# Kernel optimization log

Hardware: AMD Instinct MI355X
Metric: run time of the kernel (lower is better)

## Reference

```python
import jax, jax.numpy as jnp
import numpy as np

B, CQ, CKV, E = 8, 256, 256, 256
H, W = 64, 64
HP, WP = 32, 32


def setup_inputs() -> dict:
    key = jax.random.key(0)
    ks = jax.random.split(key, 6)
    C = jax.random.normal(ks[0], (B, CQ, H, W), dtype=jnp.float32)
    P = jax.random.normal(ks[1], (B, CKV, HP, WP), dtype=jnp.float32)
    # 1x1 conv weights, kaiming-ish scale; stored as [out_ch, in_ch]
    theta_w = jax.random.normal(ks[2], (E, CQ), dtype=jnp.float32) * (1.0 / np.sqrt(CQ))
    phi_w = jax.random.normal(ks[3], (E, CKV), dtype=jnp.float32) * (1.0 / np.sqrt(CKV))
    g_w = jax.random.normal(ks[4], (E, CKV), dtype=jnp.float32) * (1.0 / np.sqrt(CKV))
    out_w = jax.random.normal(ks[5], (CQ, E), dtype=jnp.float32) * (1.0 / np.sqrt(E))
    return {"C": C, "P": P, "theta_w": theta_w, "phi_w": phi_w, "g_w": g_w, "out_w": out_w}


def reference(C, P, theta_w, phi_w, g_w, out_w):
    b, _, h, w = C.shape
    e = theta_w.shape[0]
    # 1x1 convs are channel GEMMs
    theta_C = jnp.einsum('bchw,ec->behw', C, theta_w).reshape(b, e, h * w)   # [B,E,Nq]
    phi_P = jnp.einsum('bchw,ec->behw', P, phi_w).reshape(b, e, -1)          # [B,E,Nkv]
    g_P = jnp.einsum('bchw,ec->behw', P, g_w).reshape(b, e, -1)              # [B,E,Nkv]
    attn = jnp.einsum('ben,bem->bnm', theta_C, phi_P) / (e ** 0.5)           # [B,Nq,Nkv]
    attn = jax.nn.softmax(attn, axis=-1)
    out = jnp.einsum('bem,bnm->ben', g_P, attn).reshape(b, e, h, w)          # [B,E,H,W]
    out = jnp.einsum('behw,ce->bchw', out, out_w)                            # [B,CQ,H,W]
    return jnp.concatenate([C, out], axis=1)
```

## Files before the change

### kernel.cpp

```cpp
#include <hip/hip_runtime.h>


typedef __attribute__((ext_vector_type(8))) short short8;
typedef __attribute__((ext_vector_type(16))) float f32x16;
typedef unsigned short ushort_t;

__device__ __forceinline__ unsigned short f2bf(float f) {
    unsigned int u = __float_as_uint(f);
    u += 0x7FFFu + ((u >> 16) & 1u);
    return (unsigned short)(u >> 16);
}
__device__ __forceinline__ unsigned int pack2bf(float a, float b) {
    return (unsigned int)f2bf(a) | ((unsigned int)f2bf(b) << 16);
}
__device__ __forceinline__ void gload16(const ushort_t* g, ushort_t* l) {
    __builtin_amdgcn_global_load_lds(
        (const __attribute__((address_space(1))) unsigned int*)g,
        (__attribute__((address_space(3))) unsigned int*)l, 16, 0, 0);
}
__device__ __forceinline__ f32x16 zero16() {
    f32x16 z;
#pragma unroll
    for (int i = 0; i < 16; ++i) z[i] = 0.f;
    return z;
}

__global__ __launch_bounds__(256) void prep_w(const float* __restrict__ thw,
                                              const float* __restrict__ phw,
                                              const float* __restrict__ ow,
                                              const float* __restrict__ gw,
                                              ushort_t* __restrict__ thc,
                                              ushort_t* __restrict__ phc,
                                              ushort_t* __restrict__ w2c) {
    int blk = blockIdx.x;
    int t = threadIdx.x;
    if (blk < 64) {
        int which = blk >> 5;
        int e0 = (blk & 31) * 8;
        const float* src = which ? phw : thw;
        ushort_t* dst = which ? phc : thc;
#pragma unroll
        for (int i = 0; i < 8; ++i) {
            int e = e0 + i, c = t;
            int idx = ((((e >> 5) * 16 + (c >> 4)) * 64 + ((c >> 3) & 1) * 32 + (e & 31)) << 3) + (c & 7);
            dst[idx] = f2bf(src[e * 256 + c]);
        }
    } else {
        int c0 = (blk - 64) * 8;
        float acc[8] = {};
        for (int e = 0; e < 256; ++e) {
            float g = gw[e * 256 + t];
#pragma unroll
            for (int i = 0; i < 8; ++i) acc[i] += ow[(c0 + i) * 256 + e] * g;
        }
#pragma unroll
        for (int i = 0; i < 8; ++i) {
            int c = c0 + i, k = t;
            int idx = ((((c >> 5) * 16 + (k >> 4)) * 64 + ((k >> 3) & 1) * 32 + (c & 31)) << 3) + (k & 7);
            w2c[idx] = f2bf(acc[i]);
        }
    }
}

__global__ __launch_bounds__(256, 4) void proj_all(const ushort_t* __restrict__ thc,
                                                   const ushort_t* __restrict__ phc,
                                                   const ushort_t* __restrict__ w2c,
                                                   const float* __restrict__ C,
                                                   const float* __restrict__ P,
                                                   ushort_t* __restrict__ thetaA,
                                                   ushort_t* __restrict__ phiA,
                                                   ushort_t* __restrict__ gVx) {
    __shared__ __align__(16) ushort_t Xc[16384];
    int blk = blockIdx.x;
    int tid = threadIdx.x, lane = tid & 63, wid = tid >> 6;
    int l31 = lane & 31, lh = lane >> 5;
    const int wq = wid & 1, we = wid >> 1;

    int role, b, nt, N;
    const ushort_t* Wc;
    const float* Xg;
    ushort_t* outp;
    float scale = 1.f;
    if (blk < 512) {
        role = 0; b = blk & 7; nt = blk >> 3;
        Wc = thc; Xg = C + (size_t)b * 1048576; outp = thetaA + (size_t)b * 1048576;
        N = 4096; scale = 1.4426950408889634f / 16.0f;
    } else if (blk < 640) {
        int r = blk - 512; role = 1; b = r & 7; nt = r >> 3;
        Wc = phc; Xg = P + (size_t)b * 262144; outp = phiA + (size_t)b * 262144;
        N = 1024;
    } else {
        int r = blk - 640; role = 2; b = r & 7; nt = r >> 3;
        Wc = w2c; Xg = P + (size_t)b * 262144; outp = gVx + (size_t)b * 262144;
        N = 1024;
    }

    {
        const float* Xb = Xg + nt * 64;
        const int q = lane;
        const int sq = q >> 5, sl = q & 31;
#pragma unroll
        for (int it = 0; it < 16; ++it) {
            int ch0 = wid * 4 + it * 16;
            float v0 = Xb[(size_t)(ch0 + 0) * N + q];
            float v1 = Xb[(size_t)(ch0 + 1) * N + q];
            float v2 = Xb[(size_t)(ch0 + 2) * N + q];
            float v3 = Xb[(size_t)(ch0 + 3) * N + q];
            uint2 w;
            w.x = pack2bf(v0, v1);
            w.y = pack2bf(v2, v3);
            int ks = ch0 >> 4;
            int slh = (ch0 >> 3) & 1;
            size_t a = ((size_t)(ks * 2 + sq) * 64 + slh * 32 + sl) * 8 + (ch0 & 7);
            *(uint2*)&Xc[a] = w;
        }
    }
    __syncthreads();

    const int n0 = nt * 64 + wq * 32;
    const int ncr = (n0 >> 5) * 16;

    f32x16 o[4];
#pragma unroll
    for (int f = 0; f < 4; ++f) o[f] = zero16();

#pragma unroll
    for (int ks = 0; ks < 16; ++ks) {
        short8 xf = *(const short8*)(Xc + ((size_t)(ks * 2 + wq) * 64 + lane) * 8);
#pragma unroll
        for (int f2 = 0; f2 < 4; ++f2) {
            int f = we * 4 + f2;
            short8 wf = *(const short8*)(Wc + ((size_t)(f * 16 + ks) * 64 + lane) * 8);
            o[f2] = __builtin_amdgcn_mfma_f32_32x32x16_bf16(wf, xf, o[f2], 0, 0, 0);
        }
    }

    if (role < 2) {
#pragma unroll
        for (int f2 = 0; f2 < 4; ++f2) {
            int f = we * 4 + f2;
#pragma unroll
            for (int rq = 0; rq < 4; ++rq) {
                uint2 st;
                st.x = pack2bf(o[f2][4 * rq + 0] * scale, o[f2][4 * rq + 1] * scale);
                st.y = pack2bf(o[f2][4 * rq + 2] * scale, o[f2][4 * rq + 3] * scale);
                size_t addr = ((size_t)(ncr + f * 2 + (rq >> 1)) * 64 + l31 + 32 * (rq & 1)) * 8 + 4 * lh;
                *(uint2*)(outp + addr) = st;
            }
        }
    } else {
        int kvq = (n0 >> 4) + (l31 >> 4);
        int lhw = 32 * ((l31 >> 3) & 1);
        int kl = l31 & 7;
#pragma unroll
        for (int f2 = 0; f2 < 4; ++f2) {
            int f = we * 4 + f2;
#pragma unroll
            for (int r2 = 0; r2 < 16; ++r2) {
                int crow = (r2 & 3) + 8 * (r2 >> 2) + 4 * lh;
                size_t addr = ((size_t)(f * 64 + kvq) * 64 + crow + lhw) * 8 + kl;
                outp[addr] = f2bf(o[f2][r2]);
            }
        }
    }
}

__global__ __launch_bounds__(512, 2) void attn12(const ushort_t* __restrict__ thetaA,
                                                 const ushort_t* __restrict__ phiA,
                                                 const ushort_t* __restrict__ gVx,
                                                 const float* __restrict__ Cf,
                                                 float* __restrict__ out) {
    const int b = blockIdx.x & 7, qt = blockIdx.x >> 3;
    const int tid = threadIdx.x, lane = tid & 63, wid = tid >> 6;
    const int l31 = lane & 31, lh = lane >> 5;
    const int qg = wid & 3, z = wid >> 2;

    __shared__ __align__(16) ushort_t smem[65536];
    __shared__ __align__(16) ushort_t Pl[8192];
    __shared__ float rlS[2][4][32];

    const ushort_t* thA = thetaA + (size_t)b * 1048576;
    const ushort_t* phA = phiA + (size_t)b * 262144;
    const ushort_t* gVb = gVx + (size_t)b * 262144;

    auto stageK = [&](int j) {
        if (wid < 4) {
            const ushort_t* src = phA + (size_t)j * 16384 + (size_t)wid * 4096 + lane * 8;
            ushort_t* dst = smem + (j & 1) * 16384 + wid * 4096;
#pragma unroll
            for (int i = 0; i < 8; ++i) gload16(src + i * 512, dst + i * 512);
        }
    };
    auto stageV = [&](int j) {
        if (wid >= 4) {
            int w = wid - 4;
#pragma unroll
            for (int q2 = 0; q2 < 2; ++q2) {
                int f = w * 2 + q2;
#pragma unroll
                for (int jj = 0; jj < 4; ++jj) {
                    const ushort_t* src = gVb + ((size_t)(f * 64 + j * 4 + jj) * 64 + lane) * 8;
                    ushort_t* dst = smem + 32768 + (j & 1) * 16384 + f * 2048 + jj * 512;
                    gload16(src, dst);
                }
            }
        }
    };

    stageK(0); stageV(0);

    short8 qf[16];
    {
        const int qcr = (qt * 4 + qg) * 16;
#pragma unroll
        for (int ks = 0; ks < 16; ++ks)
            qf[ks] = *(const short8*)(thA + ((size_t)(qcr + ks) * 64 + lane) * 8);
    }

    asm volatile("s_waitcnt vmcnt(0)" ::: "memory");
    __builtin_amdgcn_s_barrier();
    __builtin_amdgcn_sched_barrier(0);
    stageK(1);

    f32x16 s = zero16();
    {
        const ushort_t* Kb = smem + z * 8192;
#pragma unroll
        for (int ks = 0; ks < 16; ++ks) {
            short8 kf = *(const short8*)(Kb + (size_t)ks * 512 + lane * 8);
            s = __builtin_amdgcn_mfma_f32_32x32x16_bf16(kf, qf[ks], s, 0, 0, 0);
        }
    }

    f32x16 o[4];
#pragma unroll
    for (int f = 0; f < 4; ++f) o[f] = zero16();
    float rl = 0.f;

    const size_t cbase = (size_t)b * 1048576 + (size_t)qt * 128 + (size_t)l31 * 4;
    const size_t dofs = (size_t)b * 1048576;
    size_t cpo = 0;
    float4 cpv;

    for (int it = 0; it < 16; ++it) {
#pragma unroll
        for (int r = 0; r < 16; ++r) s[r] = __builtin_amdgcn_exp2f(s[r]);
        float t0 = (s[0] + s[1]) + (s[2] + s[3]);
        float t1 = (s[4] + s[5]) + (s[6] + s[7]);
        float t2 = (s[8] + s[9]) + (s[10] + s[11]);
        float t3 = (s[12] + s[13]) + (s[14] + s[15]);
        float ps = (t0 + t1) + (t2 + t3);
        ps += __shfl_xor(ps, 32);
        rl += ps;

        unsigned int a0 = pack2bf(s[0], s[1]),   b0 = pack2bf(s[4], s[5]);
        unsigned int a1 = pack2bf(s[2], s[3]),   b1 = pack2bf(s[6], s[7]);
        unsigned int a2 = pack2bf(s[8], s[9]),   b2 = pack2bf(s[12], s[13]);
        unsigned int a3 = pack2bf(s[10], s[11]), b3 = pack2bf(s[14], s[15]);
        asm volatile("v_permlane32_swap_b32 %0, %1" : "+v"(a0), "+v"(b0));
        asm volatile("v_permlane32_swap_b32 %0, %1" : "+v"(a1), "+v"(b1));
        asm volatile("v_permlane32_swap_b32 %0, %1" : "+v"(a2), "+v"(b2));
        asm volatile("v_permlane32_swap_b32 %0, %1" : "+v"(a3), "+v"(b3));
        union PW { unsigned int u[4]; short8 v; };
        PW pw0, pw1;
        pw0.u[0] = a0; pw0.u[1] = a1; pw0.u[2] = b0; pw0.u[3] = b1;
        pw1.u[0] = a2; pw1.u[1] = a3; pw1.u[2] = b2; pw1.u[3] = b3;
        *(short8*)(Pl + ((size_t)(qg * 4 + 2 * z + 0) * 64 + lane) * 8) = pw0.v;
        *(short8*)(Pl + ((size_t)(qg * 4 + 2 * z + 1) * 64 + lane) * 8) = pw1.v;

        if (it == 0) asm volatile("s_waitcnt vmcnt(0)" ::: "memory");
        else         asm volatile("s_waitcnt vmcnt(1)" ::: "memory");
        asm volatile("s_waitcnt lgkmcnt(0)" ::: "memory");
        __builtin_amdgcn_s_barrier();
        __builtin_amdgcn_sched_barrier(0);

        if (it > 0) *(float4*)(out + cpo + dofs) = cpv;
        if (it < 14) stageK(it + 2);
        if (it < 15) stageV(it + 1);
        __builtin_amdgcn_sched_barrier(0);
        cpo = cbase + (size_t)(it * 16 + 2 * wid + lh) * 4096;
        cpv = *(const float4*)(Cf + cpo);

        const ushort_t* Vb = smem + 32768 + (it & 1) * 16384 + z * 8192;
        const ushort_t* Kb = smem + ((it + 1) & 1) * 16384 + z * 8192;
        __builtin_amdgcn_s_setprio(1);
        if (it < 15) {
            f32x16 sn = zero16();
#pragma unroll
            for (int j = 0; j < 4; ++j) {
                short8 pf = *(const short8*)(Pl + ((size_t)(qg * 4 + j) * 64 + lane) * 8);
#pragma unroll
                for (int fl = 0; fl < 4; ++fl) {
                    short8 vf = *(const short8*)(Vb + (size_t)fl * 2048 + j * 512 + lane * 8);
                    o[fl] = __builtin_amdgcn_mfma_f32_32x32x16_bf16(vf, pf, o[fl], 0, 0, 0);
                    int ks = j * 4 + fl;
                    short8 kf = *(const short8*)(Kb + (size_t)ks * 512 + lane * 8);
                    sn = __builtin_amdgcn_mfma_f32_32x32x16_bf16(kf, qf[ks], sn, 0, 0, 0);
                }
            }
            s = sn;
        } else {
#pragma unroll
            for (int j = 0; j < 4; ++j) {
                short8 pf = *(const short8*)(Pl + ((size_t)(qg * 4 + j) * 64 + lane) * 8);
#pragma unroll
                for (int fl = 0; fl < 4; ++fl) {
                    short8 vf = *(const short8*)(Vb + (size_t)fl * 2048 + j * 512 + lane * 8);
                    o[fl] = __builtin_amdgcn_mfma_f32_32x32x16_bf16(vf, pf, o[fl], 0, 0, 0);
                }
            }
        }
        __builtin_amdgcn_s_setprio(0);
        __builtin_amdgcn_sched_barrier(0);
        __builtin_amdgcn_s_barrier();
    }

    *(float4*)(out + cpo + dofs) = cpv;

    if (lane < 32) rlS[z][qg][l31] = rl;
    __syncthreads();
    float inv = 1.f / (rlS[0][qg][l31] + rlS[1][qg][l31]);
    float* ob = out + (size_t)b * 2097152 + (size_t)256 * 4096 + qt * 128 + qg * 32 + l31;
#pragma unroll
    for (int fl = 0; fl < 4; ++fl) {
#pragma unroll
        for (int r = 0; r < 16; ++r) {
            int e = z * 128 + fl * 32 + (r & 3) + 8 * (r >> 2) + 4 * lh;
            ob[(size_t)e * 4096] = o[fl][r] * inv;
        }
    }
}


extern "C" void kernel_launch(void* const* d_in, const int* in_sizes, int n_in,
                              void* d_out, int out_size, void* d_ws, size_t ws_size,
                              hipStream_t stream) {
    const float* C       = (const float*)d_in[0];
    const float* P       = (const float*)d_in[1];
    const float* theta_w = (const float*)d_in[2];
    const float* phi_w   = (const float*)d_in[3];
    const float* g_w     = (const float*)d_in[4];
    const float* out_w   = (const float*)d_in[5];
    float* out = (float*)d_out;

    ushort_t* ws = (ushort_t*)d_ws;
    ushort_t* thetaA = ws;
    ushort_t* phiA   = ws + 8388608;
    ushort_t* gVx    = ws + 10485760;
    ushort_t* thWc   = ws + 12582912;
    ushort_t* phWc   = ws + 12648448;
    ushort_t* w2c    = ws + 12713984;

    prep_w<<<96, 256, 0, stream>>>(theta_w, phi_w, out_w, g_w, thWc, phWc, w2c);
    proj_all<<<768, 256, 0, stream>>>(thWc, phWc, w2c, C, P, thetaA, phiA, gVx);
    attn12<<<256, 512, 0, stream>>>(thetaA, phiA, gVx, C, out);
}
```

Baseline: 105.3 us.

## Warp-specialize attention kernel into QK/softmax waves, loader waves, and split PV accumulation

The attention kernel moves from 512 to 1024 threads with specialized roles. Waves 0-7 compute QK^T scores, exp and the P tile. Waves 8-15 issue the K/V global-to-LDS staging and the C passthrough copy. All 16 waves share the PV accumulation, each owning half as many output features. This drops the software pipelining of the next QK with the current PV, splits the accumulator registers across more waves, and separates load issue from math. In exchange, QK and PV now run serially within each iteration between barriers, and occupancy drops to one 1024-thread block per CU.

```diff
diff --git a/kernel.cpp b/kernel.cpp
--- a/kernel.cpp
+++ b/kernel.cpp
@@ -165,15 +165,15 @@
     }
 }
 
-__global__ __launch_bounds__(512, 2) void attn12(const ushort_t* __restrict__ thetaA,
-                                                 const ushort_t* __restrict__ phiA,
-                                                 const ushort_t* __restrict__ gVx,
-                                                 const float* __restrict__ Cf,
-                                                 float* __restrict__ out) {
+__global__ __launch_bounds__(1024) void attn13(const ushort_t* __restrict__ thetaA,
+                                               const ushort_t* __restrict__ phiA,
+                                               const ushort_t* __restrict__ gVx,
+                                               const float* __restrict__ Cf,
+                                               float* __restrict__ out) {
     const int b = blockIdx.x & 7, qt = blockIdx.x >> 3;
     const int tid = threadIdx.x, lane = tid & 63, wid = tid >> 6;
     const int l31 = lane & 31, lh = lane >> 5;
-    const int qg = wid & 3, z = wid >> 2;
+    const int qg = wid & 3, zz = wid >> 2;
 
     __shared__ __align__(16) ushort_t smem[65536];
     __shared__ __align__(16) ushort_t Pl[8192];
@@ -184,25 +184,25 @@
     const ushort_t* gVb = gVx + (size_t)b * 262144;
 
     auto stageK = [&](int j) {
-        if (wid < 4) {
-            const ushort_t* src = phA + (size_t)j * 16384 + (size_t)wid * 4096 + lane * 8;
-            ushort_t* dst = smem + (j & 1) * 16384 + wid * 4096;
-#pragma unroll
-            for (int i = 0; i < 8; ++i) gload16(src + i * 512, dst + i * 512);
+        if (zz == 2) {
+            int w = wid - 8;
+#pragma unroll
+            for (int i = 0; i < 8; ++i) {
+                int ch = w * 8 + i;
+                const ushort_t* src = phA + (size_t)j * 16384 + (size_t)ch * 512 + lane * 8;
+                gload16(src, smem + (j & 1) * 16384 + ch * 512);
+            }
         }
     };
     auto stageV = [&](int j) {
-        if (wid >= 4) {
-            int w = wid - 4;
-#pragma unroll
-            for (int q2 = 0; q2 < 2; ++q2) {
-                int f = w * 2 + q2;
-#pragma unroll
-                for (int jj = 0; jj < 4; ++jj) {
-                    const ushort_t* src = gVb + ((size_t)(f * 64 + j * 4 + jj) * 64 + lane) * 8;
-                    ushort_t* dst = smem + 32768 + (j & 1) * 16384 + f * 2048 + jj * 512;
-                    gload16(src, dst);
-                }
+        if (zz == 3) {
+            int v = wid - 12;
+#pragma unroll
+            for (int i = 0; i < 8; ++i) {
+                int f = v * 2 + (i >> 2);
+                int kq = j * 4 + (i & 3);
+                const ushort_t* src = gVb + ((size_t)(f * 64 + kq) * 64 + lane) * 8;
+                gload16(src, smem + 32768 + (j & 1) * 16384 + f * 2048 + (i & 3) * 512);
             }
         }
     };
@@ -210,7 +210,7 @@
     stageK(0); stageV(0);
 
     short8 qf[16];
-    {
+    if (zz < 2) {
         const int qcr = (qt * 4 + qg) * 16;
 #pragma unroll
         for (int ks = 0; ks < 16; ++ks)
@@ -222,51 +222,51 @@
     __builtin_amdgcn_sched_barrier(0);
     stageK(1);
 
-    f32x16 s = zero16();
-    {
-        const ushort_t* Kb = smem + z * 8192;
-#pragma unroll
-        for (int ks = 0; ks < 16; ++ks) {
-            short8 kf = *(const short8*)(Kb + (size_t)ks * 512 + lane * 8);
-            s = __builtin_amdgcn_mfma_f32_32x32x16_bf16(kf, qf[ks], s, 0, 0, 0);
-        }
-    }
-
-    f32x16 o[4];
-#pragma unroll
-    for (int f = 0; f < 4; ++f) o[f] = zero16();
+    f32x16 o[2];
+    o[0] = zero16(); o[1] = zero16();
     float rl = 0.f;
 
-    const size_t cbase = (size_t)b * 1048576 + (size_t)qt * 128 + (size_t)l31 * 4;
+    const size_t cbase = (size_t)b * 1048576 + (size_t)qt * 128;
     const size_t dofs = (size_t)b * 1048576;
     size_t cpo = 0;
     float4 cpv;
 
     for (int it = 0; it < 16; ++it) {
-#pragma unroll
-        for (int r = 0; r < 16; ++r) s[r] = __builtin_amdgcn_exp2f(s[r]);
-        float t0 = (s[0] + s[1]) + (s[2] + s[3]);
-        float t1 = (s[4] + s[5]) + (s[6] + s[7]);
-        float t2 = (s[8] + s[9]) + (s[10] + s[11]);
-        float t3 = (s[12] + s[13]) + (s[14] + s[15]);
-        float ps = (t0 + t1) + (t2 + t3);
-        ps += __shfl_xor(ps, 32);
-        rl += ps;
-
-        unsigned int a0 = pack2bf(s[0], s[1]),   b0 = pack2bf(s[4], s[5]);
-        unsigned int a1 = pack2bf(s[2], s[3]),   b1 = pack2bf(s[6], s[7]);
-        unsigned int a2 = pack2bf(s[8], s[9]),   b2 = pack2bf(s[12], s[13]);
-        unsigned int a3 = pack2bf(s[10], s[11]), b3 = pack2bf(s[14], s[15]);
-        asm volatile("v_permlane32_swap_b32 %0, %1" : "+v"(a0), "+v"(b0));
-        asm volatile("v_permlane32_swap_b32 %0, %1" : "+v"(a1), "+v"(b1));
-        asm volatile("v_permlane32_swap_b32 %0, %1" : "+v"(a2), "+v"(b2));
-        asm volatile("v_permlane32_swap_b32 %0, %1" : "+v"(a3), "+v"(b3));
-        union PW { unsigned int u[4]; short8 v; };
-        PW pw0, pw1;
-        pw0.u[0] = a0; pw0.u[1] = a1; pw0.u[2] = b0; pw0.u[3] = b1;
-        pw1.u[0] = a2; pw1.u[1] = a3; pw1.u[2] = b2; pw1.u[3] = b3;
-        *(short8*)(Pl + ((size_t)(qg * 4 + 2 * z + 0) * 64 + lane) * 8) = pw0.v;
-        *(short8*)(Pl + ((size_t)(qg * 4 + 2 * z + 1) * 64 + lane) * 8) = pw1.v;
+        if (zz < 2) {
+            const ushort_t* Kb = smem + (it & 1) * 16384 + zz * 8192;
+            f32x16 s = zero16();
+            __builtin_amdgcn_s_setprio(1);
+#pragma unroll
+            for (int ks = 0; ks < 16; ++ks) {
+                short8 kf = *(const short8*)(Kb + (size_t)ks * 512 + lane * 8);
+                s = __builtin_amdgcn_mfma_f32_32x32x16_bf16(kf, qf[ks], s, 0, 0, 0);
+            }
+            __builtin_amdgcn_s_setprio(0);
+#pragma unroll
+            for (int r = 0; r < 16; ++r) s[r] = __builtin_amdgcn_exp2f(s[r]);
+            float t0 = (s[0] + s[1]) + (s[2] + s[3]);
+            float t1 = (s[4] + s[5]) + (s[6] + s[7]);
+            float t2 = (s[8] + s[9]) + (s[10] + s[11]);
+            float t3 = (s[12] + s[13]) + (s[14] + s[15]);
+            float ps = (t0 + t1) + (t2 + t3);
+            ps += __shfl_xor(ps, 32);
+            rl += ps;
+
+            unsigned int a0 = pack2bf(s[0], s[1]),   b0 = pack2bf(s[4], s[5]);
+            unsigned int a1 = pack2bf(s[2], s[3]),   b1 = pack2bf(s[6], s[7]);
+            unsigned int a2 = pack2bf(s[8], s[9]),   b2 = pack2bf(s[12], s[13]);
+            unsigned int a3 = pack2bf(s[10], s[11]), b3 = pack2bf(s[14], s[15]);
+            asm volatile("v_permlane32_swap_b32 %0, %1" : "+v"(a0), "+v"(b0));
+            asm volatile("v_permlane32_swap_b32 %0, %1" : "+v"(a1), "+v"(b1));
+            asm volatile("v_permlane32_swap_b32 %0, %1" : "+v"(a2), "+v"(b2));
+            asm volatile("v_permlane32_swap_b32 %0, %1" : "+v"(a3), "+v"(b3));
+            union PW { unsigned int u[4]; short8 v; };
+            PW pw0, pw1;
+            pw0.u[0] = a0; pw0.u[1] = a1; pw0.u[2] = b0; pw0.u[3] = b1;
+            pw1.u[0] = a2; pw1.u[1] = a3; pw1.u[2] = b2; pw1.u[3] = b3;
+            *(short8*)(Pl + ((size_t)(qg * 4 + 2 * zz + 0) * 64 + lane) * 8) = pw0.v;
+            *(short8*)(Pl + ((size_t)(qg * 4 + 2 * zz + 1) * 64 + lane) * 8) = pw1.v;
+        }
 
         if (it == 0) asm volatile("s_waitcnt vmcnt(0)" ::: "memory");
         else         asm volatile("s_waitcnt vmcnt(1)" ::: "memory");
@@ -274,40 +274,25 @@
         __builtin_amdgcn_s_barrier();
         __builtin_amdgcn_sched_barrier(0);
 
-        if (it > 0) *(float4*)(out + cpo + dofs) = cpv;
-        if (it < 14) stageK(it + 2);
-        if (it < 15) stageV(it + 1);
-        __builtin_amdgcn_sched_barrier(0);
-        cpo = cbase + (size_t)(it * 16 + 2 * wid + lh) * 4096;
-        cpv = *(const float4*)(Cf + cpo);
-
-        const ushort_t* Vb = smem + 32768 + (it & 1) * 16384 + z * 8192;
-        const ushort_t* Kb = smem + ((it + 1) & 1) * 16384 + z * 8192;
+        if (zz >= 2) {
+            if (it >= 1) *(float4*)(out + cpo + dofs) = cpv;
+            if (it <= 13) stageK(it + 2);
+            if (it <= 14) stageV(it + 1);
+            __builtin_amdgcn_sched_barrier(0);
+            int idx = it * 512 + (tid - 512);
+            cpo = cbase + (size_t)(idx >> 5) * 4096 + (idx & 31) * 4;
+            cpv = *(const float4*)(Cf + cpo);
+        }
+
+        const ushort_t* Vb = smem + 32768 + (it & 1) * 16384 + zz * 4096;
         __builtin_amdgcn_s_setprio(1);
-        if (it < 15) {
-            f32x16 sn = zero16();
-#pragma unroll
-            for (int j = 0; j < 4; ++j) {
-                short8 pf = *(const short8*)(Pl + ((size_t)(qg * 4 + j) * 64 + lane) * 8);
-#pragma unroll
-                for (int fl = 0; fl < 4; ++fl) {
-                    short8 vf = *(const short8*)(Vb + (size_t)fl * 2048 + j * 512 + lane * 8);
-                    o[fl] = __builtin_amdgcn_mfma_f32_32x32x16_bf16(vf, pf, o[fl], 0, 0, 0);
-                    int ks = j * 4 + fl;
-                    short8 kf = *(const short8*)(Kb + (size_t)ks * 512 + lane * 8);
-                    sn = __builtin_amdgcn_mfma_f32_32x32x16_bf16(kf, qf[ks], sn, 0, 0, 0);
-                }
-            }
-            s = sn;
-        } else {
-#pragma unroll
-            for (int j = 0; j < 4; ++j) {
-                short8 pf = *(const short8*)(Pl + ((size_t)(qg * 4 + j) * 64 + lane) * 8);
-#pragma unroll
-                for (int fl = 0; fl < 4; ++fl) {
-                    short8 vf = *(const short8*)(Vb + (size_t)fl * 2048 + j * 512 + lane * 8);
-                    o[fl] = __builtin_amdgcn_mfma_f32_32x32x16_bf16(vf, pf, o[fl], 0, 0, 0);
-                }
+#pragma unroll
+        for (int j = 0; j < 4; ++j) {
+            short8 pf = *(const short8*)(Pl + ((size_t)(qg * 4 + j) * 64 + lane) * 8);
+#pragma unroll
+            for (int fl = 0; fl < 2; ++fl) {
+                short8 vf = *(const short8*)(Vb + (size_t)fl * 2048 + j * 512 + lane * 8);
+                o[fl] = __builtin_amdgcn_mfma_f32_32x32x16_bf16(vf, pf, o[fl], 0, 0, 0);
             }
         }
         __builtin_amdgcn_s_setprio(0);
@@ -315,17 +300,17 @@
         __builtin_amdgcn_s_barrier();
     }
 
-    *(float4*)(out + cpo + dofs) = cpv;
-
-    if (lane < 32) rlS[z][qg][l31] = rl;
+    if (zz >= 2) *(float4*)(out + cpo + dofs) = cpv;
+
+    if (zz < 2 && lane < 32) rlS[zz][qg][l31] = rl;
     __syncthreads();
     float inv = 1.f / (rlS[0][qg][l31] + rlS[1][qg][l31]);
     float* ob = out + (size_t)b * 2097152 + (size_t)256 * 4096 + qt * 128 + qg * 32 + l31;
 #pragma unroll
-    for (int fl = 0; fl < 4; ++fl) {
+    for (int fl = 0; fl < 2; ++fl) {
 #pragma unroll
         for (int r = 0; r < 16; ++r) {
-            int e = z * 128 + fl * 32 + (r & 3) + 8 * (r >> 2) + 4 * lh;
+            int e = zz * 64 + fl * 32 + (r & 3) + 8 * (r >> 2) + 4 * lh;
             ob[(size_t)e * 4096] = o[fl][r] * inv;
         }
     }
@@ -353,5 +338,5 @@
 
     prep_w<<<96, 256, 0, stream>>>(theta_w, phi_w, out_w, g_w, thWc, phWc, w2c);
     proj_all<<<768, 256, 0, stream>>>(thWc, phWc, w2c, C, P, thetaA, phiA, gVx);
-    attn12<<<256, 512, 0, stream>>>(thetaA, phiA, gVx, C, out);
-}
+    attn13<<<256, 1024, 0, stream>>>(thetaA, phiA, gVx, C, out);
+}
```

Result: slower. 156.0 us (+48.2%).
